# Performance work log

Hardware: AMD Instinct MI355X
Metric: run time of the kernel (lower is better)

Reference implementation:

```python
import jax, jax.numpy as jnp
import numpy as np

HEADS = 8
DIM_K = 64
DIM_G = 64
INPLANES = 512
PLANES = 128  # int(inplanes * ratio)


def setup_inputs() -> dict:
    key = jax.random.key(0)
    ks = jax.random.split(key, 12)
    B, C, H, W = 16, INPLANES, 64, 64
    s = lambda fan: 1.0 / np.sqrt(fan)
    return {
        "x": jax.random.normal(ks[0], (B, C, H, W), dtype=jnp.float32),
        # conv_mask: Conv2d(C, HEADS, 1)
        "conv_mask_w": jax.random.normal(ks[1], (HEADS, C), dtype=jnp.float32) * s(C),
        "conv_mask_b": jnp.zeros((HEADS,), dtype=jnp.float32),
        # LinearG: dim_g -> 1
        "g_w": jax.random.normal(ks[2], (1, DIM_G), dtype=jnp.float32) * s(DIM_G),
        "g_b": jnp.zeros((1,), dtype=jnp.float32),
        # LinearK/Q/V: C -> dim_k
        "k_w": jax.random.normal(ks[3], (DIM_K, C), dtype=jnp.float32) * s(C),
        "k_b": jnp.zeros((DIM_K,), dtype=jnp.float32),
        "q_w": jax.random.normal(ks[4], (DIM_K, C), dtype=jnp.float32) * s(C),
        "q_b": jnp.zeros((DIM_K,), dtype=jnp.float32),
        "v_w": jax.random.normal(ks[5], (DIM_K, C), dtype=jnp.float32) * s(C),
        "v_b": jnp.zeros((DIM_K,), dtype=jnp.float32),
        # channel_add_conv: Conv2d(H*dk, planes, 1) -> LN([planes,1,1]) -> ReLU -> Conv2d(planes, C, 1)
        "add_w1": jax.random.normal(ks[6], (PLANES, HEADS * DIM_K), dtype=jnp.float32) * s(HEADS * DIM_K),
        "add_b1": jnp.zeros((PLANES,), dtype=jnp.float32),
        "ln_g": jnp.ones((PLANES,), dtype=jnp.float32),
        "ln_b": jnp.zeros((PLANES,), dtype=jnp.float32),
        "add_w2": jax.random.normal(ks[7], (C, PLANES), dtype=jnp.float32) * s(PLANES),
        "add_b2": jnp.zeros((C,), dtype=jnp.float32),
    }


def _forward(x, conv_mask_w, conv_mask_b, g_w, g_b, k_w, k_b, q_w, q_b,
             v_w, v_b, add_w1, add_b1, ln_g, ln_b, add_w2, add_b2):
    B, C, H, W = x.shape
    Hn, dk = HEADS, DIM_K
    # --- attention pooling mask ---
    logits = jnp.einsum('bchw,nc->bnhw', x, conv_mask_w) + conv_mask_b[None, :, None, None]
    mask = jax.nn.softmax(logits.reshape(B, Hn, H * W), axis=2)        # [B,Hn,HW]
    # per-head pooled context: [B,Hn,C]
    context = jnp.einsum('bcn,bhn->bhc', x.reshape(B, C, H * W), mask)
    # --- geometric position embedding ---
    mask4 = mask.reshape(B, Hn, H, W)
    cols = jnp.arange(W, dtype=x.dtype)   # mesh[...,0] = column index j
    rows = jnp.arange(H, dtype=x.dtype)   # mesh[...,1] = row index i
    cx = jnp.einsum('bnhw,w->bn', mask4, cols) / H
    cy = jnp.einsum('bnhw,h->bn', mask4, rows) / W
    dx = cx[:, :, None] - cx[:, None, :]
    dy = cy[:, :, None] - cy[:, None, :]
    # [B,Hn,Hn,4]
    pos = jnp.stack([jax.nn.relu(dx), jax.nn.relu(-dx),
                     jax.nn.relu(dy), jax.nn.relu(-dy)], axis=3)
    nfreq = DIM_G // 8
    dim_mat = 1.0 / (1000.0 ** (jnp.arange(nfreq, dtype=x.dtype) / nfreq))
    mul = (100.0 * pos[..., None]) * dim_mat                            # [B,Hn,Hn,4,nfreq]
    mul = mul.reshape(B, Hn, Hn, 4 * nfreq)
    emb = jnp.concatenate([jnp.sin(mul), jnp.cos(mul)], axis=-1)        # [B,Hn,Hn,DIM_G]
    w_g = jax.nn.relu(jnp.einsum('bmnd,od->bmno', emb, g_w)[..., 0] + g_b[0])  # [B,Hn,Hn]
    # --- head-level attention ---
    w_k = context @ k_w.T + k_b                                         # [B,Hn,dk]
    w_q = context @ q_w.T + q_b
    w_v = context @ v_w.T + v_b
    scaled_dot = jnp.einsum('bmd,bnd->bmn', w_k, w_q) / np.sqrt(dk)
    w_mn = jax.nn.softmax(jnp.log(jnp.clip(w_g, 1e-6)) + scaled_dot, axis=1)
    out_ctx = jnp.einsum('bmn,bmd->bnd', w_mn, w_v).reshape(B, Hn * dk)  # [B,512]
    # --- channel_add fusion (1x1 conv -> LN -> ReLU -> 1x1 conv), spatial dims are 1 ---
    y = out_ctx @ add_w1.T + add_b1                                     # [B,PLANES]
    mu = jnp.mean(y, axis=-1, keepdims=True)
    var = jnp.mean((y - mu) ** 2, axis=-1, keepdims=True)
    y = (y - mu) / jnp.sqrt(var + 1e-5) * ln_g + ln_b
    y = jax.nn.relu(y)
    add_term = y @ add_w2.T + add_b2                                    # [B,C]
    return x + add_term[:, :, None, None]


def reference(x, conv_mask_w, conv_mask_b, g_w, g_b, k_w, k_b, q_w, q_b,
              v_w, v_b, add_w1, add_b1, ln_g, ln_b, add_w2, add_b2):
    return _forward(x, conv_mask_w, conv_mask_b, g_w, g_b, k_w, k_b, q_w, q_b,
                    v_w, v_b, add_w1, add_b1, ln_g, ln_b, add_w2, add_b2)
```

## Files before the change

### kernel.cpp

```cpp
#include <hip/hip_runtime.h>
#include <cmath>

#define BB 16
#define CC 512
#define HWH 4096
#define NH 8
#define DK 64
#define PL 128

typedef float fx4 __attribute__((ext_vector_type(4)));

__device__ __forceinline__ float wred_sum(float v){
#pragma unroll
  for (int m = 32; m >= 1; m >>= 1) v += __shfl_xor(v, m, 64);
  return v;
}

__global__ __launch_bounds__(256) void k_logits(const float* __restrict__ x,
                                                const float* __restrict__ cmw,
                                                float* __restrict__ epart) {
  int bid = blockIdx.x;
  int cc = bid & 3;
  int tile = (bid >> 2) & 3;
  int b = bid >> 4;
  int p = tile * 1024 + threadIdx.x * 4;
  const float* xb = x + ((size_t)(b * CC + cc * 128)) * HWH + p;
  const float* wb = cmw + cc * 128;
  float acc[NH][4];
#pragma unroll
  for (int n = 0; n < NH; n++)
#pragma unroll
    for (int k = 0; k < 4; k++) acc[n][k] = 0.f;
#pragma unroll 4
  for (int c = 0; c < 128; c++) {
    float4 xv = *reinterpret_cast<const float4*>(xb + (size_t)c * HWH);
#pragma unroll
    for (int n = 0; n < NH; n++) {
      float w = wb[n * CC + c];
      acc[n][0] = fmaf(xv.x, w, acc[n][0]);
      acc[n][1] = fmaf(xv.y, w, acc[n][1]);
      acc[n][2] = fmaf(xv.z, w, acc[n][2]);
      acc[n][3] = fmaf(xv.w, w, acc[n][3]);
    }
  }
  float* ob = epart + (((size_t)(cc * BB + b)) * NH) * HWH + p;
#pragma unroll
  for (int n = 0; n < NH; n++) {
    float4 o = make_float4(acc[n][0], acc[n][1], acc[n][2], acc[n][3]);
    *reinterpret_cast<float4*>(ob + (size_t)n * HWH) = o;
  }
}

__global__ __launch_bounds__(256) void k_softmax(const float* __restrict__ epart,
                                                 float* __restrict__ e,
                                                 float* __restrict__ meta) {
  __shared__ float sr[4][4];
  int bn = blockIdx.x;
  int t = threadIdx.x;
  float* row = e + (size_t)bn * HWH;
  float4 v[4];
  float lmax = -1e30f;
#pragma unroll
  for (int i = 0; i < 4; i++) {
    int idx = t * 4 + i * 1024;
    const float* r = epart + (size_t)bn * HWH + idx;
    float4 a = *reinterpret_cast<const float4*>(r);
#pragma unroll
    for (int cc = 1; cc < 4; cc++) {
      float4 pth = *reinterpret_cast<const float4*>(r + (size_t)cc * BB * NH * HWH);
      a.x += pth.x; a.y += pth.y; a.z += pth.z; a.w += pth.w;
    }
    v[i] = a;
    lmax = fmaxf(lmax, fmaxf(fmaxf(a.x, a.y), fmaxf(a.z, a.w)));
  }
#pragma unroll
  for (int m = 32; m >= 1; m >>= 1) lmax = fmaxf(lmax, __shfl_xor(lmax, m, 64));
  if ((t & 63) == 0) sr[0][t >> 6] = lmax;
  __syncthreads();
  lmax = fmaxf(fmaxf(sr[0][0], sr[0][1]), fmaxf(sr[0][2], sr[0][3]));
  float s = 0.f, sc = 0.f, sy = 0.f;
#pragma unroll
  for (int i = 0; i < 4; i++) {
    int idx = t * 4 + i * 1024;
    float4 ev;
    ev.x = expf(v[i].x - lmax);
    ev.y = expf(v[i].y - lmax);
    ev.z = expf(v[i].z - lmax);
    ev.w = expf(v[i].w - lmax);
    *reinterpret_cast<float4*>(row + idx) = ev;
    float col = (float)(idx & 63);
    float rw  = (float)(idx >> 6);
    s += ev.x + ev.y + ev.z + ev.w;
    sc += ev.x * col + ev.y * (col + 1.f) + ev.z * (col + 2.f) + ev.w * (col + 3.f);
    sy += (ev.x + ev.y + ev.z + ev.w) * rw;
  }
  s = wred_sum(s); sc = wred_sum(sc); sy = wred_sum(sy);
  if ((t & 63) == 0) { sr[1][t >> 6] = s; sr[2][t >> 6] = sc; sr[3][t >> 6] = sy; }
  __syncthreads();
  if (t == 0) {
    s  = sr[1][0] + sr[1][1] + sr[1][2] + sr[1][3];
    sc = sr[2][0] + sr[2][1] + sr[2][2] + sr[2][3];
    sy = sr[3][0] + sr[3][1] + sr[3][2] + sr[3][3];
    meta[bn]       = 1.f / s;
    meta[128 + bn] = sc / (s * 64.f);
    meta[256 + bn] = sy / (s * 64.f);
  }
}

__global__ __launch_bounds__(512) void k_context(const float* __restrict__ x,
                                                 const float* __restrict__ e,
                                                 float* __restrict__ pctx) {
  int bid = blockIdx.x;
  int ng = bid & 1;
  int cg = (bid >> 1) & 15;
  int b = bid >> 5;
  int w = threadIdx.x >> 6;
  int l = threadIdx.x & 63;
  int cbase = cg * 32 + w * 4;
  const float* xb = x + ((size_t)(b * CC + cbase)) * HWH + ng * 2048 + l * 4;
  const float* eb = e + (size_t)b * NH * HWH + ng * 2048 + l * 4;
  float acc[4][NH];
#pragma unroll
  for (int ci = 0; ci < 4; ci++)
#pragma unroll
    for (int h = 0; h < NH; h++) acc[ci][h] = 0.f;

#pragma unroll 2
  for (int ch = 0; ch < 8; ch++) {
    int off = ch * 256;
    float4 ev[NH];
#pragma unroll
    for (int h = 0; h < NH; h++)
      ev[h] = *reinterpret_cast<const float4*>(eb + (size_t)h * HWH + off);
#pragma unroll
    for (int ci = 0; ci < 4; ci++) {
      float4 xv = *reinterpret_cast<const float4*>(xb + (size_t)ci * HWH + off);
#pragma unroll
      for (int h = 0; h < NH; h++) {
        float a = acc[ci][h];
        a = fmaf(xv.x, ev[h].x, a);
        a = fmaf(xv.y, ev[h].y, a);
        a = fmaf(xv.z, ev[h].z, a);
        a = fmaf(xv.w, ev[h].w, a);
        acc[ci][h] = a;
      }
    }
  }
#pragma unroll
  for (int ci = 0; ci < 4; ci++)
#pragma unroll
    for (int h = 0; h < NH; h++) acc[ci][h] = wred_sum(acc[ci][h]);
  if (l == 0) {
    float* op = pctx + (((size_t)(ng * BB + b)) * NH) * CC + cbase;
#pragma unroll
    for (int h = 0; h < NH; h++)
#pragma unroll
      for (int ci = 0; ci < 4; ci++) op[h * CC + ci] = acc[ci][h];
  }
}

__global__ __launch_bounds__(512) void k_kqv(const float* __restrict__ pctx,
    const float* __restrict__ meta,
    const float* __restrict__ k_w, const float* __restrict__ q_w,
    const float* __restrict__ v_w,
    const float* __restrict__ k_b, const float* __restrict__ q_b,
    const float* __restrict__ v_b,
    float* __restrict__ kqvbuf) {
  int bid = blockIdx.x;
  int b = bid / 24;
  int r = bid - b * 24;
  int j = r >> 3;
  int h = r & 7;
  int t = threadIdx.x;
  __shared__ float ctx[8 * 68];
  __shared__ float psum[64][9];
  float inv = meta[b * NH + h];
  size_t base = ((size_t)b * NH + h) * CC + t;
  float cval = (pctx[base] + pctx[(size_t)BB * NH * CC + base]) * inv;
  ctx[(t >> 6) * 68 + (t & 63)] = cval;
  __syncthreads();
  const float* wm = (j == 0) ? k_w : (j == 1) ? q_w : v_w;
  const float* bm = (j == 0) ? k_b : (j == 1) ? q_b : v_b;
  int d = t >> 3, s = t & 7;
  const float* wr = wm + d * CC + s * 64;
  const float* cl = ctx + s * 68;
  float a = 0.f;
#pragma unroll
  for (int c = 0; c < 64; c += 4) {
    float4 w4 = *reinterpret_cast<const float4*>(wr + c);
    a = fmaf(w4.x, cl[c + 0], a);
    a = fmaf(w4.y, cl[c + 1], a);
    a = fmaf(w4.z, cl[c + 2], a);
    a = fmaf(w4.w, cl[c + 3], a);
  }
  psum[d][s] = a;
  __syncthreads();
  if (t < 64) {
    float rsum = 0.f;
#pragma unroll
    for (int ss = 0; ss < 8; ss++) rsum += psum[t][ss];
    kqvbuf[((size_t)(b * 3 + j) * NH + h) * DK + t] = rsum + bm[t];
  }
}

__global__ __launch_bounds__(512) void k_attn_mlp(const float* __restrict__ kqvbuf,
    const float* __restrict__ meta,
    const float* __restrict__ g_w, const float* __restrict__ g_b,
    const float* __restrict__ aw1, const float* __restrict__ ab1,
    const float* __restrict__ lng, const float* __restrict__ lnb,
    const float* __restrict__ aw2, const float* __restrict__ ab2,
    float* __restrict__ add_term) {
  int b = blockIdx.x;
  int t = threadIdx.x;
  __shared__ float kq[3][NH * 68];
  __shared__ float smn[NH][NH];
  __shared__ float cxl[NH], cyl[NH];
  __shared__ float oc[CC];
  __shared__ float part[4][PL];
  __shared__ float yl[PL];
  __shared__ float sr[2][2];

  if (t < NH) { cxl[t] = meta[128 + b * NH + t]; cyl[t] = meta[256 + b * NH + t]; }
  {
    int h = t >> 6, d = t & 63;
#pragma unroll
    for (int j = 0; j < 3; j++)
      kq[j][h * 68 + d] = kqvbuf[(size_t)(b * 3 + j) * 512 + t];
  }
  __syncthreads();

  if (t < 64) {
    int m = t >> 3, n = t & 7;
    float dx = cxl[m] - cxl[n];
    float dy = cyl[m] - cyl[n];
    float pos[4] = { fmaxf(dx, 0.f), fmaxf(-dx, 0.f), fmaxf(dy, 0.f), fmaxf(-dy, 0.f) };
    float a = g_b[0];
#pragma unroll
    for (int p = 0; p < 4; p++) {
#pragma unroll
      for (int f = 0; f < 8; f++) {
        float dm = expf(-0.8634694098727671f * (float)f);
        float ang = 100.f * pos[p] * dm;
        a = fmaf(sinf(ang), g_w[p * 8 + f], a);
        a = fmaf(cosf(ang), g_w[32 + p * 8 + f], a);
      }
    }
    float wgl = logf(fmaxf(fmaxf(a, 0.f), 1e-6f));
    float dot = 0.f;
#pragma unroll
    for (int dd = 0; dd < DK; dd++)
      dot = fmaf(kq[0][m * 68 + dd], kq[1][n * 68 + dd], dot);
    smn[m][n] = dot * 0.125f + wgl;
  }
  __syncthreads();
  if (t < 8) {
    float mx = -1e30f;
#pragma unroll
    for (int m = 0; m < NH; m++) mx = fmaxf(mx, smn[m][t]);
    float ssum = 0.f; float ex[NH];
#pragma unroll
    for (int m = 0; m < NH; m++) { ex[m] = expf(smn[m][t] - mx); ssum += ex[m]; }
#pragma unroll
    for (int m = 0; m < NH; m++) smn[m][t] = ex[m] / ssum;
  }
  __syncthreads();
  {
    int n = t >> 6, d = t & 63;
    float a = 0.f;
#pragma unroll
    for (int m = 0; m < NH; m++) a = fmaf(smn[m][n], kq[2][m * 68 + d], a);
    oc[t] = a;
  }
  __syncthreads();
  {
    int d = t & 127, p = t >> 7;
    const float* wr = aw1 + d * CC + p * 128;
    const float* ol = oc + p * 128;
    float a = 0.f;
#pragma unroll 8
    for (int c = 0; c < 128; c += 4) {
      float4 w4 = *reinterpret_cast<const float4*>(wr + c);
      a = fmaf(w4.x, ol[c + 0], a);
      a = fmaf(w4.y, ol[c + 1], a);
      a = fmaf(w4.z, ol[c + 2], a);
      a = fmaf(w4.w, ol[c + 3], a);
    }
    part[p][d] = a;
  }
  __syncthreads();
  float y = 0.f;
  if (t < PL) y = part[0][t] + part[1][t] + part[2][t] + part[3][t] + ab1[t];
  {
    float s  = (t < PL) ? y : 0.f;
    float sq = s * y;
    s = wred_sum(s); sq = wred_sum(sq);
    if (t < PL && (t & 63) == 0) { sr[0][t >> 6] = s; sr[1][t >> 6] = sq; }
  }
  __syncthreads();
  {
    float mu = (sr[0][0] + sr[0][1]) * (1.f / 128.f);
    float var = (sr[1][0] + sr[1][1]) * (1.f / 128.f) - mu * mu;
    float rstd = rsqrtf(var + 1e-5f);
    if (t < PL) yl[t] = fmaxf((y - mu) * rstd * lng[t] + lnb[t], 0.f);
  }
  __syncthreads();
  {
    const float* wr = aw2 + t * PL;
    float a = ab2[t];
#pragma unroll 8
    for (int pp = 0; pp < PL; pp += 4) {
      float4 w4 = *reinterpret_cast<const float4*>(wr + pp);
      a = fmaf(w4.x, yl[pp + 0], a);
      a = fmaf(w4.y, yl[pp + 1], a);
      a = fmaf(w4.z, yl[pp + 2], a);
      a = fmaf(w4.w, yl[pp + 3], a);
    }
    add_term[b * CC + t] = a;
  }
}

__global__ __launch_bounds__(256) void k_add(const float* __restrict__ x,
                                             const float* __restrict__ add_term,
                                             float* __restrict__ out) {
  const fx4* x4 = reinterpret_cast<const fx4*>(x);
  fx4* o4 = reinterpret_cast<fx4*>(out);
  const size_t n4 = (size_t)BB * CC * HWH / 4;
  for (size_t i = (size_t)blockIdx.x * 256 + threadIdx.x; i < n4;
       i += (size_t)gridDim.x * 256) {
    fx4 v = x4[i];
    float a = add_term[i >> 10];
    v += a;
    __builtin_nontemporal_store(v, &o4[i]);
  }
}

extern "C" void kernel_launch(void* const* d_in, const int* in_sizes, int n_in,
                              void* d_out, int out_size, void* d_ws, size_t ws_size,
                              hipStream_t stream) {
  const float* x   = (const float*)d_in[0];
  const float* cmw = (const float*)d_in[1];
  const float* g_w = (const float*)d_in[3];
  const float* g_b = (const float*)d_in[4];
  const float* k_w = (const float*)d_in[5];
  const float* k_b = (const float*)d_in[6];
  const float* q_w = (const float*)d_in[7];
  const float* q_b = (const float*)d_in[8];
  const float* v_w = (const float*)d_in[9];
  const float* v_b = (const float*)d_in[10];
  const float* aw1 = (const float*)d_in[11];
  const float* ab1 = (const float*)d_in[12];
  const float* lng = (const float*)d_in[13];
  const float* lnb = (const float*)d_in[14];
  const float* aw2 = (const float*)d_in[15];
  const float* ab2 = (const float*)d_in[16];
  float* out = (float*)d_out;
  float* ws = (float*)d_ws;

  float* epart    = ws;
  float* e        = ws + 2097152;
  float* meta     = ws + 2621440;
  float* pctx     = ws;
  float* kqvbuf   = ws + 131072;
  float* add_term = ws + 155648;

  hipLaunchKernelGGL(k_logits,   dim3(256),  dim3(256), 0, stream, x, cmw, epart);
  hipLaunchKernelGGL(k_softmax,  dim3(128),  dim3(256), 0, stream, epart, e, meta);
  hipLaunchKernelGGL(k_context,  dim3(512),  dim3(512), 0, stream, x, e, pctx);
  hipLaunchKernelGGL(k_kqv,      dim3(384),  dim3(512), 0, stream, pctx, meta,
                     k_w, q_w, v_w, k_b, q_b, v_b, kqvbuf);
  hipLaunchKernelGGL(k_attn_mlp, dim3(16),   dim3(512), 0, stream, kqvbuf, meta,
                     g_w, g_b, aw1, ab1, lng, lnb, aw2, ab2, add_term);
  hipLaunchKernelGGL(k_add,      dim3(2048), dim3(256), 0, stream, x, add_term, out);
}
```

Before: 163.1 us.

## Fuse all six stages into one persistent kernel with grid-wide barriers

Replaces the six separate launches with a single 256-block, 1024-thread persistent kernel that separates stages with atomic-counter global barriers, zeroed by a memset before each launch. Work partitioning is reshaped: the logits stage now splits channels 16 ways, so the softmax stage has to reduce 16 partial sums. This is meant to remove launch overhead and inter-kernel gaps. The cost is spin-wait barrier latency, idle blocks in the small stages, and a risk of deadlock if all 256 blocks are not co-resident.

```diff
diff --git a/kernel.cpp b/kernel.cpp
--- a/kernel.cpp
+++ b/kernel.cpp
@@ -7,6 +7,8 @@
 #define NH 8
 #define DK 64
 #define PL 128
+#define NBLK 256
+#define NTHR 1024
 
 typedef float fx4 __attribute__((ext_vector_type(4)));
 
@@ -15,322 +17,339 @@
   for (int m = 32; m >= 1; m >>= 1) v += __shfl_xor(v, m, 64);
   return v;
 }
-
-__global__ __launch_bounds__(256) void k_logits(const float* __restrict__ x,
-                                                const float* __restrict__ cmw,
-                                                float* __restrict__ epart) {
-  int bid = blockIdx.x;
-  int cc = bid & 3;
-  int tile = (bid >> 2) & 3;
-  int b = bid >> 4;
-  int p = tile * 1024 + threadIdx.x * 4;
-  const float* xb = x + ((size_t)(b * CC + cc * 128)) * HWH + p;
-  const float* wb = cmw + cc * 128;
-  float acc[NH][4];
-#pragma unroll
-  for (int n = 0; n < NH; n++)
-#pragma unroll
-    for (int k = 0; k < 4; k++) acc[n][k] = 0.f;
-#pragma unroll 4
-  for (int c = 0; c < 128; c++) {
-    float4 xv = *reinterpret_cast<const float4*>(xb + (size_t)c * HWH);
-#pragma unroll
-    for (int n = 0; n < NH; n++) {
-      float w = wb[n * CC + c];
-      acc[n][0] = fmaf(xv.x, w, acc[n][0]);
-      acc[n][1] = fmaf(xv.y, w, acc[n][1]);
-      acc[n][2] = fmaf(xv.z, w, acc[n][2]);
-      acc[n][3] = fmaf(xv.w, w, acc[n][3]);
-    }
-  }
-  float* ob = epart + (((size_t)(cc * BB + b)) * NH) * HWH + p;
-#pragma unroll
-  for (int n = 0; n < NH; n++) {
-    float4 o = make_float4(acc[n][0], acc[n][1], acc[n][2], acc[n][3]);
-    *reinterpret_cast<float4*>(ob + (size_t)n * HWH) = o;
-  }
-}
-
-__global__ __launch_bounds__(256) void k_softmax(const float* __restrict__ epart,
-                                                 float* __restrict__ e,
-                                                 float* __restrict__ meta) {
-  __shared__ float sr[4][4];
-  int bn = blockIdx.x;
-  int t = threadIdx.x;
-  float* row = e + (size_t)bn * HWH;
-  float4 v[4];
-  float lmax = -1e30f;
-#pragma unroll
-  for (int i = 0; i < 4; i++) {
-    int idx = t * 4 + i * 1024;
-    const float* r = epart + (size_t)bn * HWH + idx;
-    float4 a = *reinterpret_cast<const float4*>(r);
-#pragma unroll
-    for (int cc = 1; cc < 4; cc++) {
-      float4 pth = *reinterpret_cast<const float4*>(r + (size_t)cc * BB * NH * HWH);
-      a.x += pth.x; a.y += pth.y; a.z += pth.z; a.w += pth.w;
-    }
-    v[i] = a;
-    lmax = fmaxf(lmax, fmaxf(fmaxf(a.x, a.y), fmaxf(a.z, a.w)));
-  }
-#pragma unroll
-  for (int m = 32; m >= 1; m >>= 1) lmax = fmaxf(lmax, __shfl_xor(lmax, m, 64));
-  if ((t & 63) == 0) sr[0][t >> 6] = lmax;
+__device__ __forceinline__ float wred_max(float v){
+#pragma unroll
+  for (int m = 32; m >= 1; m >>= 1) v = fmaxf(v, __shfl_xor(v, m, 64));
+  return v;
+}
+
+__device__ __forceinline__ void gbar(int* bar, int id) {
   __syncthreads();
-  lmax = fmaxf(fmaxf(sr[0][0], sr[0][1]), fmaxf(sr[0][2], sr[0][3]));
-  float s = 0.f, sc = 0.f, sy = 0.f;
-#pragma unroll
-  for (int i = 0; i < 4; i++) {
-    int idx = t * 4 + i * 1024;
-    float4 ev;
-    ev.x = expf(v[i].x - lmax);
-    ev.y = expf(v[i].y - lmax);
-    ev.z = expf(v[i].z - lmax);
-    ev.w = expf(v[i].w - lmax);
-    *reinterpret_cast<float4*>(row + idx) = ev;
-    float col = (float)(idx & 63);
-    float rw  = (float)(idx >> 6);
-    s += ev.x + ev.y + ev.z + ev.w;
-    sc += ev.x * col + ev.y * (col + 1.f) + ev.z * (col + 2.f) + ev.w * (col + 3.f);
-    sy += (ev.x + ev.y + ev.z + ev.w) * rw;
-  }
-  s = wred_sum(s); sc = wred_sum(sc); sy = wred_sum(sy);
-  if ((t & 63) == 0) { sr[1][t >> 6] = s; sr[2][t >> 6] = sc; sr[3][t >> 6] = sy; }
+  if (threadIdx.x == 0) {
+    __threadfence();
+    __hip_atomic_fetch_add(bar + id, 1, __ATOMIC_ACQ_REL, __HIP_MEMORY_SCOPE_AGENT);
+    while (__hip_atomic_load(bar + id, __ATOMIC_ACQUIRE, __HIP_MEMORY_SCOPE_AGENT) < NBLK)
+      __builtin_amdgcn_s_sleep(8);
+    __threadfence();
+  }
   __syncthreads();
-  if (t == 0) {
-    s  = sr[1][0] + sr[1][1] + sr[1][2] + sr[1][3];
-    sc = sr[2][0] + sr[2][1] + sr[2][2] + sr[2][3];
-    sy = sr[3][0] + sr[3][1] + sr[3][2] + sr[3][3];
-    meta[bn]       = 1.f / s;
-    meta[128 + bn] = sc / (s * 64.f);
-    meta[256 + bn] = sy / (s * 64.f);
-  }
-}
-
-__global__ __launch_bounds__(512) void k_context(const float* __restrict__ x,
-                                                 const float* __restrict__ e,
-                                                 float* __restrict__ pctx) {
-  int bid = blockIdx.x;
-  int ng = bid & 1;
-  int cg = (bid >> 1) & 15;
-  int b = bid >> 5;
-  int w = threadIdx.x >> 6;
-  int l = threadIdx.x & 63;
-  int cbase = cg * 32 + w * 4;
-  const float* xb = x + ((size_t)(b * CC + cbase)) * HWH + ng * 2048 + l * 4;
-  const float* eb = e + (size_t)b * NH * HWH + ng * 2048 + l * 4;
-  float acc[4][NH];
-#pragma unroll
-  for (int ci = 0; ci < 4; ci++)
-#pragma unroll
-    for (int h = 0; h < NH; h++) acc[ci][h] = 0.f;
-
-#pragma unroll 2
-  for (int ch = 0; ch < 8; ch++) {
-    int off = ch * 256;
-    float4 ev[NH];
-#pragma unroll
-    for (int h = 0; h < NH; h++)
-      ev[h] = *reinterpret_cast<const float4*>(eb + (size_t)h * HWH + off);
-#pragma unroll
-    for (int ci = 0; ci < 4; ci++) {
-      float4 xv = *reinterpret_cast<const float4*>(xb + (size_t)ci * HWH + off);
-#pragma unroll
-      for (int h = 0; h < NH; h++) {
-        float a = acc[ci][h];
-        a = fmaf(xv.x, ev[h].x, a);
-        a = fmaf(xv.y, ev[h].y, a);
-        a = fmaf(xv.z, ev[h].z, a);
-        a = fmaf(xv.w, ev[h].w, a);
-        acc[ci][h] = a;
-      }
-    }
-  }
-#pragma unroll
-  for (int ci = 0; ci < 4; ci++)
-#pragma unroll
-    for (int h = 0; h < NH; h++) acc[ci][h] = wred_sum(acc[ci][h]);
-  if (l == 0) {
-    float* op = pctx + (((size_t)(ng * BB + b)) * NH) * CC + cbase;
-#pragma unroll
-    for (int h = 0; h < NH; h++)
-#pragma unroll
-      for (int ci = 0; ci < 4; ci++) op[h * CC + ci] = acc[ci][h];
-  }
-}
-
-__global__ __launch_bounds__(512) void k_kqv(const float* __restrict__ pctx,
-    const float* __restrict__ meta,
-    const float* __restrict__ k_w, const float* __restrict__ q_w,
-    const float* __restrict__ v_w,
-    const float* __restrict__ k_b, const float* __restrict__ q_b,
-    const float* __restrict__ v_b,
-    float* __restrict__ kqvbuf) {
-  int bid = blockIdx.x;
-  int b = bid / 24;
-  int r = bid - b * 24;
-  int j = r >> 3;
-  int h = r & 7;
-  int t = threadIdx.x;
-  __shared__ float ctx[8 * 68];
-  __shared__ float psum[64][9];
-  float inv = meta[b * NH + h];
-  size_t base = ((size_t)b * NH + h) * CC + t;
-  float cval = (pctx[base] + pctx[(size_t)BB * NH * CC + base]) * inv;
-  ctx[(t >> 6) * 68 + (t & 63)] = cval;
-  __syncthreads();
-  const float* wm = (j == 0) ? k_w : (j == 1) ? q_w : v_w;
-  const float* bm = (j == 0) ? k_b : (j == 1) ? q_b : v_b;
-  int d = t >> 3, s = t & 7;
-  const float* wr = wm + d * CC + s * 64;
-  const float* cl = ctx + s * 68;
-  float a = 0.f;
-#pragma unroll
-  for (int c = 0; c < 64; c += 4) {
-    float4 w4 = *reinterpret_cast<const float4*>(wr + c);
-    a = fmaf(w4.x, cl[c + 0], a);
-    a = fmaf(w4.y, cl[c + 1], a);
-    a = fmaf(w4.z, cl[c + 2], a);
-    a = fmaf(w4.w, cl[c + 3], a);
-  }
-  psum[d][s] = a;
-  __syncthreads();
-  if (t < 64) {
-    float rsum = 0.f;
-#pragma unroll
-    for (int ss = 0; ss < 8; ss++) rsum += psum[t][ss];
-    kqvbuf[((size_t)(b * 3 + j) * NH + h) * DK + t] = rsum + bm[t];
-  }
-}
-
-__global__ __launch_bounds__(512) void k_attn_mlp(const float* __restrict__ kqvbuf,
-    const float* __restrict__ meta,
+}
+
+#define OFF_EPART 0
+#define OFF_E     8388608
+#define OFF_META  8912896
+#define OFF_BAR   8913408
+#define OFF_PCTX  8913920
+#define OFF_KQV   9044992
+#define OFF_ADDT  9069568
+
+__global__ __launch_bounds__(NTHR) void k_fused(
+    const float* __restrict__ x, const float* __restrict__ cmw,
     const float* __restrict__ g_w, const float* __restrict__ g_b,
+    const float* __restrict__ k_w, const float* __restrict__ k_b,
+    const float* __restrict__ q_w, const float* __restrict__ q_b,
+    const float* __restrict__ v_w, const float* __restrict__ v_b,
     const float* __restrict__ aw1, const float* __restrict__ ab1,
     const float* __restrict__ lng, const float* __restrict__ lnb,
     const float* __restrict__ aw2, const float* __restrict__ ab2,
-    float* __restrict__ add_term) {
-  int b = blockIdx.x;
-  int t = threadIdx.x;
-  __shared__ float kq[3][NH * 68];
-  __shared__ float smn[NH][NH];
-  __shared__ float cxl[NH], cyl[NH];
-  __shared__ float oc[CC];
-  __shared__ float part[4][PL];
-  __shared__ float yl[PL];
-  __shared__ float sr[2][2];
-
-  if (t < NH) { cxl[t] = meta[128 + b * NH + t]; cyl[t] = meta[256 + b * NH + t]; }
+    float* __restrict__ out, float* __restrict__ ws) {
+  __shared__ float smem[4096];
+  float* epart = ws + OFF_EPART;
+  float* e     = ws + OFF_E;
+  float* meta  = ws + OFF_META;
+  int*   bar   = (int*)(ws + OFF_BAR);
+  float* pctx  = ws + OFF_PCTX;
+  float* kqvb  = ws + OFF_KQV;
+  float* addt  = ws + OFF_ADDT;
+
+  const int bid = blockIdx.x;
+  const int t = threadIdx.x;
+  const int w = t >> 6, l = t & 63;
+
   {
-    int h = t >> 6, d = t & 63;
-#pragma unroll
-    for (int j = 0; j < 3; j++)
-      kq[j][h * 68 + d] = kqvbuf[(size_t)(b * 3 + j) * 512 + t];
-  }
-  __syncthreads();
-
-  if (t < 64) {
-    int m = t >> 3, n = t & 7;
-    float dx = cxl[m] - cxl[n];
-    float dy = cyl[m] - cyl[n];
-    float pos[4] = { fmaxf(dx, 0.f), fmaxf(-dx, 0.f), fmaxf(dy, 0.f), fmaxf(-dy, 0.f) };
-    float a = g_b[0];
-#pragma unroll
-    for (int p = 0; p < 4; p++) {
-#pragma unroll
-      for (int f = 0; f < 8; f++) {
-        float dm = expf(-0.8634694098727671f * (float)f);
-        float ang = 100.f * pos[p] * dm;
-        a = fmaf(sinf(ang), g_w[p * 8 + f], a);
-        a = fmaf(cosf(ang), g_w[32 + p * 8 + f], a);
-      }
-    }
-    float wgl = logf(fmaxf(fmaxf(a, 0.f), 1e-6f));
-    float dot = 0.f;
-#pragma unroll
-    for (int dd = 0; dd < DK; dd++)
-      dot = fmaf(kq[0][m * 68 + dd], kq[1][n * 68 + dd], dot);
-    smn[m][n] = dot * 0.125f + wgl;
-  }
-  __syncthreads();
-  if (t < 8) {
-    float mx = -1e30f;
-#pragma unroll
-    for (int m = 0; m < NH; m++) mx = fmaxf(mx, smn[m][t]);
-    float ssum = 0.f; float ex[NH];
-#pragma unroll
-    for (int m = 0; m < NH; m++) { ex[m] = expf(smn[m][t] - mx); ssum += ex[m]; }
-#pragma unroll
-    for (int m = 0; m < NH; m++) smn[m][t] = ex[m] / ssum;
-  }
-  __syncthreads();
+    int b = bid >> 4, cc = bid & 15;
+    int p = t * 4;
+    const float* xb = x + ((size_t)(b * CC + cc * 32)) * HWH + p;
+    const float* wb = cmw + cc * 32;
+    float acc[NH][4];
+#pragma unroll
+    for (int n = 0; n < NH; n++)
+#pragma unroll
+      for (int k = 0; k < 4; k++) acc[n][k] = 0.f;
+#pragma unroll 8
+    for (int c = 0; c < 32; c++) {
+      float4 xv = *reinterpret_cast<const float4*>(xb + (size_t)c * HWH);
+#pragma unroll
+      for (int n = 0; n < NH; n++) {
+        float wv = wb[n * CC + c];
+        acc[n][0] = fmaf(xv.x, wv, acc[n][0]);
+        acc[n][1] = fmaf(xv.y, wv, acc[n][1]);
+        acc[n][2] = fmaf(xv.z, wv, acc[n][2]);
+        acc[n][3] = fmaf(xv.w, wv, acc[n][3]);
+      }
+    }
+    float* ob = epart + ((size_t)(cc * BB + b) * NH) * HWH + p;
+#pragma unroll
+    for (int n = 0; n < NH; n++)
+      *reinterpret_cast<float4*>(ob + (size_t)n * HWH) =
+          make_float4(acc[n][0], acc[n][1], acc[n][2], acc[n][3]);
+  }
+  gbar(bar, 0);
+
+  if (bid < 128) {
+    int row = bid;
+    int p = t * 4;
+    const float* rp = epart + (size_t)row * HWH + p;
+    float4 a = *reinterpret_cast<const float4*>(rp);
+#pragma unroll
+    for (int sub = 1; sub < 16; sub++) {
+      float4 q = *reinterpret_cast<const float4*>(rp + (size_t)sub * (BB * NH * HWH));
+      a.x += q.x; a.y += q.y; a.z += q.z; a.w += q.w;
+    }
+    float m = fmaxf(fmaxf(a.x, a.y), fmaxf(a.z, a.w));
+    m = wred_max(m);
+    if (l == 0) smem[w] = m;
+    __syncthreads();
+    if (t == 0) {
+      float mm = smem[0];
+#pragma unroll
+      for (int i = 1; i < 16; i++) mm = fmaxf(mm, smem[i]);
+      smem[16] = mm;
+    }
+    __syncthreads();
+    m = smem[16];
+    float4 ev;
+    ev.x = expf(a.x - m); ev.y = expf(a.y - m);
+    ev.z = expf(a.z - m); ev.w = expf(a.w - m);
+    *reinterpret_cast<float4*>(e + (size_t)row * HWH + p) = ev;
+    float s = ev.x + ev.y + ev.z + ev.w;
+    float col = (float)(p & 63);
+    float sc = ev.x * col + ev.y * (col + 1.f) + ev.z * (col + 2.f) + ev.w * (col + 3.f);
+    float sy = s * (float)(p >> 6);
+    s = wred_sum(s); sc = wred_sum(sc); sy = wred_sum(sy);
+    __syncthreads();
+    if (l == 0) { smem[w] = s; smem[16 + w] = sc; smem[32 + w] = sy; }
+    __syncthreads();
+    if (t == 0) {
+      float S = 0.f, SC = 0.f, SY = 0.f;
+#pragma unroll
+      for (int i = 0; i < 16; i++) { S += smem[i]; SC += smem[16 + i]; SY += smem[32 + i]; }
+      meta[row]       = 1.f / S;
+      meta[128 + row] = SC / (S * 64.f);
+      meta[256 + row] = SY / (S * 64.f);
+    }
+  }
+  gbar(bar, 1);
+
   {
-    int n = t >> 6, d = t & 63;
-    float a = 0.f;
-#pragma unroll
-    for (int m = 0; m < NH; m++) a = fmaf(smn[m][n], kq[2][m * 68 + d], a);
-    oc[t] = a;
-  }
-  __syncthreads();
+    int ng = bid & 1;
+    int g2 = bid >> 1;
+    int b = g2 >> 3, cg8 = g2 & 7;
+    int cbase = cg8 * 64 + w * 4;
+    const float* xb = x + ((size_t)(b * CC + cbase)) * HWH + ng * 2048 + l * 4;
+    const float* eb = e + (size_t)b * NH * HWH + ng * 2048 + l * 4;
+    float acc[4][NH];
+#pragma unroll
+    for (int ci = 0; ci < 4; ci++)
+#pragma unroll
+      for (int h = 0; h < NH; h++) acc[ci][h] = 0.f;
+#pragma unroll 2
+    for (int ch = 0; ch < 8; ch++) {
+      int off = ch * 256;
+      float4 ev[NH];
+#pragma unroll
+      for (int h = 0; h < NH; h++)
+        ev[h] = *reinterpret_cast<const float4*>(eb + (size_t)h * HWH + off);
+#pragma unroll
+      for (int ci = 0; ci < 4; ci++) {
+        float4 xv = *reinterpret_cast<const float4*>(xb + (size_t)ci * HWH + off);
+#pragma unroll
+        for (int h = 0; h < NH; h++) {
+          float a = acc[ci][h];
+          a = fmaf(xv.x, ev[h].x, a);
+          a = fmaf(xv.y, ev[h].y, a);
+          a = fmaf(xv.z, ev[h].z, a);
+          a = fmaf(xv.w, ev[h].w, a);
+          acc[ci][h] = a;
+        }
+      }
+    }
+#pragma unroll
+    for (int ci = 0; ci < 4; ci++)
+#pragma unroll
+      for (int h = 0; h < NH; h++) acc[ci][h] = wred_sum(acc[ci][h]);
+    if (l == 0) {
+      float* op = pctx + ((size_t)(ng * BB + b) * NH) * CC + cbase;
+#pragma unroll
+      for (int h = 0; h < NH; h++)
+#pragma unroll
+        for (int ci = 0; ci < 4; ci++) op[h * CC + ci] = acc[ci][h];
+    }
+  }
+  gbar(bar, 2);
+
+  if (bid < 192) {
+    int b = bid / 12;
+    int r = bid - b * 12;
+#pragma unroll
+    for (int uu = 0; uu < 2; uu++) {
+      int u = r * 2 + uu;
+      int j = u >> 3, h = u & 7;
+      const float* wm = (j == 0) ? k_w : (j == 1) ? q_w : v_w;
+      const float* bm = (j == 0) ? k_b : (j == 1) ? q_b : v_b;
+      if (t < 512) {
+        float val = (pctx[((size_t)(0 * BB + b) * NH + h) * CC + t] +
+                     pctx[((size_t)(1 * BB + b) * NH + h) * CC + t]) * meta[b * NH + h];
+        smem[(t >> 5) * 33 + (t & 31)] = val;
+      }
+      __syncthreads();
+      {
+        int d = t >> 4, s4 = t & 15;
+        const float* wr = wm + d * CC + s4 * 32;
+        const float* cl = smem + s4 * 33;
+        float a = 0.f;
+#pragma unroll
+        for (int c = 0; c < 32; c += 4) {
+          float4 w4 = *reinterpret_cast<const float4*>(wr + c);
+          a = fmaf(w4.x, cl[c + 0], a);
+          a = fmaf(w4.y, cl[c + 1], a);
+          a = fmaf(w4.z, cl[c + 2], a);
+          a = fmaf(w4.w, cl[c + 3], a);
+        }
+        smem[544 + d * 17 + s4] = a;
+      }
+      __syncthreads();
+      if (t < 64) {
+        float rs = 0.f;
+#pragma unroll
+        for (int ss = 0; ss < 16; ss++) rs += smem[544 + t * 17 + ss];
+        kqvb[((size_t)(b * 3 + j) * NH + h) * DK + t] = rs + bm[t];
+      }
+      __syncthreads();
+    }
+  }
+  gbar(bar, 3);
+
+  if (bid < BB) {
+    int b = bid;
+    float* kq   = smem;
+    float* smn  = smem + 1632;
+    float* cxl  = smem + 1696;
+    float* cyl  = smem + 1704;
+    float* oc   = smem + 1712;
+    float* part = smem + 2224;
+    float* yl   = smem + 2736;
+    float* srr  = smem + 2864;
+    if (t < NH) { cxl[t] = meta[128 + b * NH + t]; cyl[t] = meta[256 + b * NH + t]; }
+    if (t < 512) {
+      int h = t >> 6, d = t & 63;
+#pragma unroll
+      for (int j = 0; j < 3; j++)
+        kq[j * 544 + h * 68 + d] = kqvb[(size_t)(b * 3 + j) * 512 + t];
+    }
+    __syncthreads();
+    if (t < 64) {
+      int m = t >> 3, n = t & 7;
+      float dx = cxl[m] - cxl[n];
+      float dy = cyl[m] - cyl[n];
+      float pos[4] = { fmaxf(dx, 0.f), fmaxf(-dx, 0.f), fmaxf(dy, 0.f), fmaxf(-dy, 0.f) };
+      float a = g_b[0];
+#pragma unroll
+      for (int p = 0; p < 4; p++) {
+#pragma unroll
+        for (int f = 0; f < 8; f++) {
+          float dm = expf(-0.8634694098727671f * (float)f);
+          float ang = 100.f * pos[p] * dm;
+          a = fmaf(sinf(ang), g_w[p * 8 + f], a);
+          a = fmaf(cosf(ang), g_w[32 + p * 8 + f], a);
+        }
+      }
+      float wgl = logf(fmaxf(fmaxf(a, 0.f), 1e-6f));
+      float dot = 0.f;
+#pragma unroll
+      for (int dd = 0; dd < DK; dd++)
+        dot = fmaf(kq[m * 68 + dd], kq[544 + n * 68 + dd], dot);
+      smn[m * 8 + n] = dot * 0.125f + wgl;
+    }
+    __syncthreads();
+    if (t < 8) {
+      float mx = -1e30f;
+#pragma unroll
+      for (int m = 0; m < NH; m++) mx = fmaxf(mx, smn[m * 8 + t]);
+      float ssum = 0.f; float ex[NH];
+#pragma unroll
+      for (int m = 0; m < NH; m++) { ex[m] = expf(smn[m * 8 + t] - mx); ssum += ex[m]; }
+#pragma unroll
+      for (int m = 0; m < NH; m++) smn[m * 8 + t] = ex[m] / ssum;
+    }
+    __syncthreads();
+    if (t < 512) {
+      int n = t >> 6, d = t & 63;
+      float a = 0.f;
+#pragma unroll
+      for (int m = 0; m < NH; m++) a = fmaf(smn[m * 8 + n], kq[2 * 544 + m * 68 + d], a);
+      oc[t] = a;
+    }
+    __syncthreads();
+    if (t < 512) {
+      int d = t & 127, pq = t >> 7;
+      const float* wr = aw1 + d * CC + pq * 128;
+      const float* ol = oc + pq * 128;
+      float a = 0.f;
+#pragma unroll 8
+      for (int c = 0; c < 128; c += 4) {
+        float4 w4 = *reinterpret_cast<const float4*>(wr + c);
+        a = fmaf(w4.x, ol[c + 0], a);
+        a = fmaf(w4.y, ol[c + 1], a);
+        a = fmaf(w4.z, ol[c + 2], a);
+        a = fmaf(w4.w, ol[c + 3], a);
+      }
+      part[pq * 128 + d] = a;
+    }
+    __syncthreads();
+    float y = 0.f;
+    if (t < PL) y = part[t] + part[128 + t] + part[256 + t] + part[384 + t] + ab1[t];
+    {
+      float s  = (t < PL) ? y : 0.f;
+      float sq = s * y;
+      s = wred_sum(s); sq = wred_sum(sq);
+      if (t < PL && l == 0) { srr[w] = s; srr[2 + w] = sq; }
+    }
+    __syncthreads();
+    {
+      float mu = (srr[0] + srr[1]) * (1.f / 128.f);
+      float var = (srr[2] + srr[3]) * (1.f / 128.f) - mu * mu;
+      float rstd = rsqrtf(var + 1e-5f);
+      if (t < PL) yl[t] = fmaxf((y - mu) * rstd * lng[t] + lnb[t], 0.f);
+    }
+    __syncthreads();
+    if (t < 512) {
+      const float* wr = aw2 + t * PL;
+      float a = ab2[t];
+#pragma unroll 8
+      for (int pp = 0; pp < PL; pp += 4) {
+        float4 w4 = *reinterpret_cast<const float4*>(wr + pp);
+        a = fmaf(w4.x, yl[pp + 0], a);
+        a = fmaf(w4.y, yl[pp + 1], a);
+        a = fmaf(w4.z, yl[pp + 2], a);
+        a = fmaf(w4.w, yl[pp + 3], a);
+      }
+      addt[b * CC + t] = a;
+    }
+  }
+  gbar(bar, 4);
+
   {
-    int d = t & 127, p = t >> 7;
-    const float* wr = aw1 + d * CC + p * 128;
-    const float* ol = oc + p * 128;
-    float a = 0.f;
-#pragma unroll 8
-    for (int c = 0; c < 128; c += 4) {
-      float4 w4 = *reinterpret_cast<const float4*>(wr + c);
-      a = fmaf(w4.x, ol[c + 0], a);
-      a = fmaf(w4.y, ol[c + 1], a);
-      a = fmaf(w4.z, ol[c + 2], a);
-      a = fmaf(w4.w, ol[c + 3], a);
-    }
-    part[p][d] = a;
-  }
-  __syncthreads();
-  float y = 0.f;
-  if (t < PL) y = part[0][t] + part[1][t] + part[2][t] + part[3][t] + ab1[t];
-  {
-    float s  = (t < PL) ? y : 0.f;
-    float sq = s * y;
-    s = wred_sum(s); sq = wred_sum(sq);
-    if (t < PL && (t & 63) == 0) { sr[0][t >> 6] = s; sr[1][t >> 6] = sq; }
-  }
-  __syncthreads();
-  {
-    float mu = (sr[0][0] + sr[0][1]) * (1.f / 128.f);
-    float var = (sr[1][0] + sr[1][1]) * (1.f / 128.f) - mu * mu;
-    float rstd = rsqrtf(var + 1e-5f);
-    if (t < PL) yl[t] = fmaxf((y - mu) * rstd * lng[t] + lnb[t], 0.f);
-  }
-  __syncthreads();
-  {
-    const float* wr = aw2 + t * PL;
-    float a = ab2[t];
-#pragma unroll 8
-    for (int pp = 0; pp < PL; pp += 4) {
-      float4 w4 = *reinterpret_cast<const float4*>(wr + pp);
-      a = fmaf(w4.x, yl[pp + 0], a);
-      a = fmaf(w4.y, yl[pp + 1], a);
-      a = fmaf(w4.z, yl[pp + 2], a);
-      a = fmaf(w4.w, yl[pp + 3], a);
-    }
-    add_term[b * CC + t] = a;
-  }
-}
-
-__global__ __launch_bounds__(256) void k_add(const float* __restrict__ x,
-                                             const float* __restrict__ add_term,
-                                             float* __restrict__ out) {
-  const fx4* x4 = reinterpret_cast<const fx4*>(x);
-  fx4* o4 = reinterpret_cast<fx4*>(out);
-  const size_t n4 = (size_t)BB * CC * HWH / 4;
-  for (size_t i = (size_t)blockIdx.x * 256 + threadIdx.x; i < n4;
-       i += (size_t)gridDim.x * 256) {
-    fx4 v = x4[i];
-    float a = add_term[i >> 10];
-    v += a;
-    __builtin_nontemporal_store(v, &o4[i]);
+    const fx4* x4 = reinterpret_cast<const fx4*>(x);
+    fx4* o4 = reinterpret_cast<fx4*>(out);
+    size_t base = (size_t)bid * NTHR + t;
+#pragma unroll 4
+    for (int it = 0; it < 32; it++) {
+      size_t i = base + (size_t)it * (NBLK * NTHR);
+      fx4 v = x4[i];
+      v += addt[i >> 10];
+      __builtin_nontemporal_store(v, &o4[i]);
+    }
   }
 }
 
@@ -356,19 +375,8 @@
   float* out = (float*)d_out;
   float* ws = (float*)d_ws;
 
-  float* epart    = ws;
-  float* e        = ws + 2097152;
-  float* meta     = ws + 2621440;
-  float* pctx     = ws;
-  float* kqvbuf   = ws + 131072;
-  float* add_term = ws + 155648;
-
-  hipLaunchKernelGGL(k_logits,   dim3(256),  dim3(256), 0, stream, x, cmw, epart);
-  hipLaunchKernelGGL(k_softmax,  dim3(128),  dim3(256), 0, stream, epart, e, meta);
-  hipLaunchKernelGGL(k_context,  dim3(512),  dim3(512), 0, stream, x, e, pctx);
-  hipLaunchKernelGGL(k_kqv,      dim3(384),  dim3(512), 0, stream, pctx, meta,
-                     k_w, q_w, v_w, k_b, q_b, v_b, kqvbuf);
-  hipLaunchKernelGGL(k_attn_mlp, dim3(16),   dim3(512), 0, stream, kqvbuf, meta,
-                     g_w, g_b, aw1, ab1, lng, lnb, aw2, ab2, add_term);
-  hipLaunchKernelGGL(k_add,      dim3(2048), dim3(256), 0, stream, x, add_term, out);
-}
+  hipMemsetAsync(ws + OFF_BAR, 0, 64, stream);
+  hipLaunchKernelGGL(k_fused, dim3(NBLK), dim3(NTHR), 0, stream,
+                     x, cmw, g_w, g_b, k_w, k_b, q_w, q_b, v_w, v_b,
+                     aw1, ab1, lng, lnb, aw2, ab2, out, ws);
+}
```

After: 315.8 us. +93.6%, slower.
